# Kernel optimization log

Hardware: AMD Instinct MI355X
Metric: run time of the kernel (lower is better)

The kernel has to match this reference:

```python
import jax, jax.numpy as jnp
import numpy as np

NEG = -1e9  # matches torch masked_fill value (additive, not -inf)

def setup_inputs() -> dict:
    key = jax.random.key(0)
    k1, k2, k3, k4 = jax.random.split(key, 4)
    B, H, S, D = 8, 16, 1024, 64
    q = jax.random.normal(k1, (B, H, S, D), dtype=jnp.float32)
    k = jax.random.normal(k2, (B, H, S, D), dtype=jnp.float32)
    v = jax.random.normal(k3, (B, H, S, D), dtype=jnp.float32)
    event_length = jax.random.randint(k4, (B,), 0, S, dtype=jnp.int32)
    return {"q": q, "k": k, "v": v, "event_length": event_length}

def reference(q, k, v, event_length):
    B, H, S, D = q.shape
    scale = 1.0 / jnp.sqrt(jnp.asarray(D, dtype=q.dtype))
    idx = jnp.arange(S)
    # valid[b, i] = i < event_length[b]
    valid = idx[None, :] < event_length[:, None]            # [B, S]
    # additive mask: 0 where (row valid AND col valid), else -1e9
    pair = valid[:, :, None] & valid[:, None, :]            # [B, S, S]
    attn_mask = jnp.where(pair, 0.0, NEG).astype(q.dtype)[:, None, :, :]  # [B,1,S,S]
    scores = jnp.einsum('bhqd,bhkd->bhqk', q, k) * scale + attn_mask
    probs = jax.nn.softmax(scores, axis=-1)
    out = jnp.einsum('bhqk,bhkd->bhqd', probs, v)
    return out
```

## Files before the change

### kernel.cpp

```cpp
#include <hip/hip_runtime.h>


#define Sdim 1024
#define Ddim 64
#define PITCH 72

typedef float f32x4 __attribute__((ext_vector_type(4)));
typedef _Float16 f16x8 __attribute__((ext_vector_type(8)));
typedef unsigned short u16x8 __attribute__((ext_vector_type(8)));
typedef unsigned int u32x2 __attribute__((ext_vector_type(2)));

union FragU { u16x8 u; f16x8 h; };

__device__ __forceinline__ unsigned pk2(float a, float b) {
  auto h = __builtin_amdgcn_cvt_pkrtz(a, b);
  return __builtin_bit_cast(unsigned, h);
}

__device__ __forceinline__ float fexp2(float x) {
  float r;
  asm("v_exp_f32 %0, %1" : "=v"(r) : "v"(x));
  return r;
}

__global__ __launch_bounds__(256, 3)
void attn_fwd(const float* __restrict__ Q, const float* __restrict__ K,
              const float* __restrict__ V, const int* __restrict__ EL,
              float* __restrict__ Out) {
  __shared__ unsigned short k_lds[64 * PITCH];
  __shared__ unsigned short v_lds[64 * PITCH];
  __shared__ unsigned short p_lds[4][32 * PITCH];

  const int bid0 = blockIdx.x;
  const int x  = bid0 & 7;
  const int j  = bid0 >> 3;
  const int c  = j & 31;
  const int t  = j >> 5;
  const int p  = (c >> 2) + 8 * (t >> 1);
  const int i4 = c & 3;
  const int qt = (t & 1) ? (7 - i4) : i4;
  const int bh = p * 8 + x;
  const int L  = EL[bh >> 4];

  const int tid  = threadIdx.x;
  const size_t base = (size_t)bh * Sdim * Ddim;
  const float* Qb = Q + base;
  const float* Kb = K + base;
  const float* Vb = V + base;

  const int q0blk = qt * 128;

  if (q0blk >= L) {
    float* red = (float*)k_lds;
    const int sc4 = (tid & 15) * 4;
    const int rg0 = tid >> 4;
    const float* vp = Vb + (size_t)rg0 * Ddim + sc4;
    float4 acc = {0.f, 0.f, 0.f, 0.f};
#pragma unroll 8
    for (int i = 0; i < 64; ++i) {
      float4 a = *(const float4*)(vp + (size_t)i * 16 * Ddim);
      acc.x += a.x; acc.y += a.y; acc.z += a.z; acc.w += a.w;
    }
    *(float4*)&red[rg0 * 68 + sc4] = acc;
    __syncthreads();
    if (tid < 16) {
      float4 s = {0.f, 0.f, 0.f, 0.f};
#pragma unroll
      for (int i = 0; i < 16; ++i) {
        float4 a = *(const float4*)&red[i * 68 + tid * 4];
        s.x += a.x; s.y += a.y; s.z += a.z; s.w += a.w;
      }
      const float inv = 1.0f / 1024.0f;
      s.x *= inv; s.y *= inv; s.z *= inv; s.w *= inv;
      *(float4*)&red[16 * 68 + tid * 4] = s;
    }
    __syncthreads();
    const float4 cm = *(const float4*)&red[16 * 68 + sc4];
    float* ob = Out + base;
#pragma unroll
    for (int pp = 0; pp < 8; ++pp) {
      int row = q0blk + pp * 16 + rg0;
      *(float4*)&ob[(size_t)row * Ddim + sc4] = cm;
    }
    return;
  }

  const int w    = tid >> 6;
  const int lane = tid & 63;
  const int r    = lane & 15;
  const int hi   = lane >> 4;

  const int q0w      = q0blk + w * 32;
  const bool wValid  = q0w < L;
  const bool wAllVal = (q0w + 32) <= L;
  const int kFull    = (L + 63) >> 6;
  const int ktB      = L >> 6;

  const bool qv0 = (q0w + r) < L;
  const bool qv1 = (q0w + 16 + r) < L;
  const bool straddle = (q0blk + 128) > L;

  const float SCL = 0.125f * 1.44269504088896340736f;
  f16x8 qf[2][2];
  if (wValid) {
#pragma unroll
    for (int qc = 0; qc < 2; ++qc)
#pragma unroll
      for (int kk = 0; kk < 2; ++kk) {
        const float* pq = Qb + (size_t)(q0w + qc * 16 + r) * Ddim + kk * 32 + hi * 8;
        float4 a = *(const float4*)pq;
        float4 cc = *(const float4*)(pq + 4);
        union { unsigned u[4]; f16x8 h; } f;
        f.u[0] = pk2(a.x * SCL, a.y * SCL);  f.u[1] = pk2(a.z * SCL, a.w * SCL);
        f.u[2] = pk2(cc.x * SCL, cc.y * SCL); f.u[3] = pk2(cc.z * SCL, cc.w * SCL);
        qf[qc][kk] = f.h;
      }
  }

  const f32x4 zero4 = {0.f, 0.f, 0.f, 0.f};
  f32x4 oacc[2][4];
#pragma unroll
  for (int qc = 0; qc < 2; ++qc)
#pragma unroll
    for (int dc = 0; dc < 4; ++dc) oacc[qc][dc] = zero4;

  float lpart[2] = {0.f, 0.f};

  const int sr = tid >> 4, sc = tid & 15;
  const float* pK = Kb + (size_t)sr * Ddim + sc * 4;
  const float* pV = Vb + (size_t)(sr * 4) * Ddim + sc * 4;

  float4 kpre[4], vpre[4];
  auto LOADK = [&](int k0_) {
#pragma unroll
    for (int i = 0; i < 4; ++i)
      kpre[i] = *(const float4*)(pK + (size_t)(k0_ + 16 * i) * Ddim);
  };
  auto LOADV = [&](int k0_) {
#pragma unroll
    for (int jj = 0; jj < 4; ++jj)
      vpre[jj] = *(const float4*)(pV + (size_t)(k0_ + jj) * Ddim);
  };

  LOADK(0);
  LOADV(0);

  for (int kt = 0; kt < kFull; ++kt) {
    const int k0 = kt * 64;
    __syncthreads();

#pragma unroll
    for (int i = 0; i < 4; ++i) {
      u32x2 o;
      o[0] = pk2(kpre[i].x, kpre[i].y); o[1] = pk2(kpre[i].z, kpre[i].w);
      *(u32x2*)&k_lds[(16 * i + sr) * PITCH + sc * 4] = o;
    }
    {
      u32x2 o;
      o[0] = pk2(vpre[0].x, vpre[1].x); o[1] = pk2(vpre[2].x, vpre[3].x);
      *(u32x2*)&v_lds[(sc * 4 + 0) * PITCH + sr * 4] = o;
      o[0] = pk2(vpre[0].y, vpre[1].y); o[1] = pk2(vpre[2].y, vpre[3].y);
      *(u32x2*)&v_lds[(sc * 4 + 1) * PITCH + sr * 4] = o;
      o[0] = pk2(vpre[0].z, vpre[1].z); o[1] = pk2(vpre[2].z, vpre[3].z);
      *(u32x2*)&v_lds[(sc * 4 + 2) * PITCH + sr * 4] = o;
      o[0] = pk2(vpre[0].w, vpre[1].w); o[1] = pk2(vpre[2].w, vpre[3].w);
      *(u32x2*)&v_lds[(sc * 4 + 3) * PITCH + sr * 4] = o;
    }
    __syncthreads();

    if (kt + 1 < kFull) { LOADK(k0 + 64); LOADV(k0 + 64); }

    if (wValid) {
      f32x4 sacc[2][4];
#pragma unroll
      for (int qc = 0; qc < 2; ++qc)
#pragma unroll
        for (int kc = 0; kc < 4; ++kc) sacc[qc][kc] = zero4;

      __builtin_amdgcn_s_setprio(1);
#pragma unroll
      for (int kc = 0; kc < 4; ++kc)
#pragma unroll
        for (int kk = 0; kk < 2; ++kk) {
          FragU kf;
          kf.u = *(const u16x8*)&k_lds[(kc * 16 + r) * PITCH + kk * 32 + hi * 8];
          sacc[0][kc] = __builtin_amdgcn_mfma_f32_16x16x32_f16(kf.h, qf[0][kk], sacc[0][kc], 0, 0, 0);
          sacc[1][kc] = __builtin_amdgcn_mfma_f32_16x16x32_f16(kf.h, qf[1][kk], sacc[1][kc], 0, 0, 0);
        }
      __builtin_amdgcn_s_setprio(0);

      const bool noMask = wAllVal && (kt != ktB);
#pragma unroll
      for (int qc = 0; qc < 2; ++qc) {
        const bool qv = qc ? qv1 : qv0;
        float ls = 0.f;
#pragma unroll
        for (int kc = 0; kc < 4; ++kc) {
          float pr[4];
#pragma unroll
          for (int rg = 0; rg < 4; ++rg) {
            float s = sacc[qc][kc][rg];
            if (!noMask) {
              int kg = k0 + kc * 16 + 4 * hi + rg;
              s = (qv && kg < L) ? s : -__builtin_inff();
            }
            pr[rg] = fexp2(s);
            ls += pr[rg];
          }
          u32x2 o;
          o[0] = pk2(pr[0], pr[1]);
          o[1] = pk2(pr[2], pr[3]);
          *(u32x2*)&p_lds[w][(qc * 16 + r) * PITCH + kc * 16 + 4 * hi] = o;
        }
        lpart[qc] += ls;
      }

      asm volatile("s_waitcnt lgkmcnt(0)" ::: "memory");
      __builtin_amdgcn_sched_barrier(0);

      __builtin_amdgcn_s_setprio(1);
#pragma unroll
      for (int ks = 0; ks < 2; ++ks) {
        FragU pf0, pf1;
        pf0.u = *(const u16x8*)&p_lds[w][(0  + r) * PITCH + ks * 32 + hi * 8];
        pf1.u = *(const u16x8*)&p_lds[w][(16 + r) * PITCH + ks * 32 + hi * 8];
#pragma unroll
        for (int dc = 0; dc < 4; ++dc) {
          FragU vf;
          vf.u = *(const u16x8*)&v_lds[(dc * 16 + r) * PITCH + ks * 32 + hi * 8];
          oacc[0][dc] = __builtin_amdgcn_mfma_f32_16x16x32_f16(pf0.h, vf.h, oacc[0][dc], 0, 0, 0);
          oacc[1][dc] = __builtin_amdgcn_mfma_f32_16x16x32_f16(pf1.h, vf.h, oacc[1][dc], 0, 0, 0);
        }
      }
      __builtin_amdgcn_s_setprio(0);
    }
  }

  float* ob = Out + base;
#pragma unroll
  for (int qc = 0; qc < 2; ++qc) {
    float l = lpart[qc];
    l += __shfl_xor(l, 16, 64);
    l += __shfl_xor(l, 32, 64);
#pragma unroll
    for (int rg = 0; rg < 4; ++rg) {
      float lsq = __shfl(l, 4 * hi + rg, 64);
      float inv = 1.0f / lsq;
      int qrow = q0w + qc * 16 + 4 * hi + rg;
      if (qrow < L) {
#pragma unroll
        for (int dc = 0; dc < 4; ++dc)
          ob[(size_t)qrow * Ddim + dc * 16 + r] = oacc[qc][dc][rg] * inv;
      }
    }
  }

  if (straddle) {
    __syncthreads();
    float* red = (float*)k_lds;
    const int sc4 = (tid & 15) * 4;
    const int rg0 = tid >> 4;
    const float* vp = Vb + (size_t)rg0 * Ddim + sc4;
    float4 acc = {0.f, 0.f, 0.f, 0.f};
#pragma unroll 8
    for (int i = 0; i < 64; ++i) {
      float4 a = *(const float4*)(vp + (size_t)i * 16 * Ddim);
      acc.x += a.x; acc.y += a.y; acc.z += a.z; acc.w += a.w;
    }
    *(float4*)&red[rg0 * 68 + sc4] = acc;
    __syncthreads();
    if (tid < 16) {
      float4 s = {0.f, 0.f, 0.f, 0.f};
#pragma unroll
      for (int i = 0; i < 16; ++i) {
        float4 a = *(const float4*)&red[i * 68 + tid * 4];
        s.x += a.x; s.y += a.y; s.z += a.z; s.w += a.w;
      }
      const float inv = 1.0f / 1024.0f;
      s.x *= inv; s.y *= inv; s.z *= inv; s.w *= inv;
      *(float4*)&red[16 * 68 + tid * 4] = s;
    }
    __syncthreads();
    const float4 cm = *(const float4*)&red[16 * 68 + sc4];
#pragma unroll
    for (int pp = 0; pp < 8; ++pp) {
      int row = q0blk + pp * 16 + rg0;
      if (row >= L)
        *(float4*)&ob[(size_t)row * Ddim + sc4] = cm;
    }
  }
}

extern "C" void kernel_launch(void* const* d_in, const int* in_sizes, int n_in,
                              void* d_out, int out_size, void* d_ws, size_t ws_size,
                              hipStream_t stream) {
  const float* q  = (const float*)d_in[0];
  const float* k  = (const float*)d_in[1];
  const float* v  = (const float*)d_in[2];
  const int*   el = (const int*)d_in[3];
  float* out = (float*)d_out;
  dim3 grid(8 * 16 * (Sdim / 128));
  dim3 block(256);
  hipLaunchKernelGGL(attn_fwd, grid, block, 0, stream, q, k, v, el, out);
}
```

Measured before the change: 46.58 us.

## Halve query tile to 64 rows with 2-wave blocks and swizzle V LDS layout

Measured after the change: 51.29 us. 10.1% more time.

```diff
diff --git a/kernel.cpp b/kernel.cpp
--- a/kernel.cpp
+++ b/kernel.cpp
@@ -23,24 +23,21 @@
   return r;
 }
 
-__global__ __launch_bounds__(256, 3)
+__global__ __launch_bounds__(128, 2)
 void attn_fwd(const float* __restrict__ Q, const float* __restrict__ K,
               const float* __restrict__ V, const int* __restrict__ EL,
               float* __restrict__ Out) {
   __shared__ unsigned short k_lds[64 * PITCH];
   __shared__ unsigned short v_lds[64 * PITCH];
-  __shared__ unsigned short p_lds[4][32 * PITCH];
+  __shared__ unsigned short p_lds[2][32 * PITCH];
 
   const int bid0 = blockIdx.x;
-  const int x  = bid0 & 7;
-  const int j  = bid0 >> 3;
-  const int c  = j & 31;
-  const int t  = j >> 5;
-  const int p  = (c >> 2) + 8 * (t >> 1);
-  const int i4 = c & 3;
-  const int qt = (t & 1) ? (7 - i4) : i4;
-  const int bh = p * 8 + x;
-  const int L  = EL[bh >> 4];
+  const int x   = bid0 & 7;
+  const int j   = bid0 >> 3;
+  const int pan = j >> 4;
+  const int qt  = j & 15;
+  const int bh  = pan * 8 + x;
+  const int L   = EL[bh >> 4];
 
   const int tid  = threadIdx.x;
   const size_t base = (size_t)bh * Sdim * Ddim;
@@ -48,7 +45,7 @@
   const float* Kb = K + base;
   const float* Vb = V + base;
 
-  const int q0blk = qt * 128;
+  const int q0blk = qt * 64;
 
   if (q0blk >= L) {
     float* red = (float*)k_lds;
@@ -57,8 +54,8 @@
     const float* vp = Vb + (size_t)rg0 * Ddim + sc4;
     float4 acc = {0.f, 0.f, 0.f, 0.f};
 #pragma unroll 8
-    for (int i = 0; i < 64; ++i) {
-      float4 a = *(const float4*)(vp + (size_t)i * 16 * Ddim);
+    for (int i = 0; i < 128; ++i) {
+      float4 a = *(const float4*)(vp + (size_t)i * 8 * Ddim);
       acc.x += a.x; acc.y += a.y; acc.z += a.z; acc.w += a.w;
     }
     *(float4*)&red[rg0 * 68 + sc4] = acc;
@@ -66,20 +63,20 @@
     if (tid < 16) {
       float4 s = {0.f, 0.f, 0.f, 0.f};
 #pragma unroll
-      for (int i = 0; i < 16; ++i) {
+      for (int i = 0; i < 8; ++i) {
         float4 a = *(const float4*)&red[i * 68 + tid * 4];
         s.x += a.x; s.y += a.y; s.z += a.z; s.w += a.w;
       }
       const float inv = 1.0f / 1024.0f;
       s.x *= inv; s.y *= inv; s.z *= inv; s.w *= inv;
-      *(float4*)&red[16 * 68 + tid * 4] = s;
-    }
-    __syncthreads();
-    const float4 cm = *(const float4*)&red[16 * 68 + sc4];
+      *(float4*)&red[8 * 68 + tid * 4] = s;
+    }
+    __syncthreads();
+    const float4 cm = *(const float4*)&red[8 * 68 + sc4];
     float* ob = Out + base;
 #pragma unroll
     for (int pp = 0; pp < 8; ++pp) {
-      int row = q0blk + pp * 16 + rg0;
+      int row = q0blk + pp * 8 + rg0;
       *(float4*)&ob[(size_t)row * Ddim + sc4] = cm;
     }
     return;
@@ -89,16 +86,17 @@
   const int lane = tid & 63;
   const int r    = lane & 15;
   const int hi   = lane >> 4;
+  const int r3   = r >> 3;
 
   const int q0w      = q0blk + w * 32;
   const bool wValid  = q0w < L;
   const bool wAllVal = (q0w + 32) <= L;
   const int kFull    = (L + 63) >> 6;
   const int ktB      = L >> 6;
+  const bool straddle = (q0blk + 64) > L;
 
   const bool qv0 = (q0w + r) < L;
   const bool qv1 = (q0w + 16 + r) < L;
-  const bool straddle = (q0blk + 128) > L;
 
   const float SCL = 0.125f * 1.44269504088896340736f;
   f16x8 qf[2][2];
@@ -111,7 +109,7 @@
         float4 a = *(const float4*)pq;
         float4 cc = *(const float4*)(pq + 4);
         union { unsigned u[4]; f16x8 h; } f;
-        f.u[0] = pk2(a.x * SCL, a.y * SCL);  f.u[1] = pk2(a.z * SCL, a.w * SCL);
+        f.u[0] = pk2(a.x * SCL, a.y * SCL);   f.u[1] = pk2(a.z * SCL, a.w * SCL);
         f.u[2] = pk2(cc.x * SCL, cc.y * SCL); f.u[3] = pk2(cc.z * SCL, cc.w * SCL);
         qf[qc][kk] = f.h;
       }
@@ -126,20 +124,24 @@
 
   float lpart[2] = {0.f, 0.f};
 
-  const int sr = tid >> 4, sc = tid & 15;
+  const int sr = tid >> 4;
+  const int sc = tid & 15;
+  const int vskew = ((sc >> 1) & 7) * 8;
   const float* pK = Kb + (size_t)sr * Ddim + sc * 4;
   const float* pV = Vb + (size_t)(sr * 4) * Ddim + sc * 4;
 
-  float4 kpre[4], vpre[4];
+  float4 kpre[8], vpre[8];
   auto LOADK = [&](int k0_) {
 #pragma unroll
-    for (int i = 0; i < 4; ++i)
-      kpre[i] = *(const float4*)(pK + (size_t)(k0_ + 16 * i) * Ddim);
+    for (int i = 0; i < 8; ++i)
+      kpre[i] = *(const float4*)(pK + (size_t)(k0_ + 8 * i) * Ddim);
   };
   auto LOADV = [&](int k0_) {
 #pragma unroll
-    for (int jj = 0; jj < 4; ++jj)
-      vpre[jj] = *(const float4*)(pV + (size_t)(k0_ + jj) * Ddim);
+    for (int j2 = 0; j2 < 2; ++j2)
+#pragma unroll
+      for (int jj = 0; jj < 4; ++jj)
+        vpre[j2 * 4 + jj] = *(const float4*)(pV + (size_t)(k0_ + 32 * j2 + jj) * Ddim);
   };
 
   LOADK(0);
@@ -150,21 +152,23 @@
     __syncthreads();
 
 #pragma unroll
-    for (int i = 0; i < 4; ++i) {
+    for (int i = 0; i < 8; ++i) {
       u32x2 o;
       o[0] = pk2(kpre[i].x, kpre[i].y); o[1] = pk2(kpre[i].z, kpre[i].w);
-      *(u32x2*)&k_lds[(16 * i + sr) * PITCH + sc * 4] = o;
-    }
-    {
+      *(u32x2*)&k_lds[(8 * i + sr) * PITCH + sc * 4] = o;
+    }
+#pragma unroll
+    for (int j2 = 0; j2 < 2; ++j2) {
+      const int cp = (sr * 4 + 32 * j2 + vskew) & 63;
       u32x2 o;
-      o[0] = pk2(vpre[0].x, vpre[1].x); o[1] = pk2(vpre[2].x, vpre[3].x);
-      *(u32x2*)&v_lds[(sc * 4 + 0) * PITCH + sr * 4] = o;
-      o[0] = pk2(vpre[0].y, vpre[1].y); o[1] = pk2(vpre[2].y, vpre[3].y);
-      *(u32x2*)&v_lds[(sc * 4 + 1) * PITCH + sr * 4] = o;
-      o[0] = pk2(vpre[0].z, vpre[1].z); o[1] = pk2(vpre[2].z, vpre[3].z);
-      *(u32x2*)&v_lds[(sc * 4 + 2) * PITCH + sr * 4] = o;
-      o[0] = pk2(vpre[0].w, vpre[1].w); o[1] = pk2(vpre[2].w, vpre[3].w);
-      *(u32x2*)&v_lds[(sc * 4 + 3) * PITCH + sr * 4] = o;
+      o[0] = pk2(vpre[4*j2+0].x, vpre[4*j2+1].x); o[1] = pk2(vpre[4*j2+2].x, vpre[4*j2+3].x);
+      *(u32x2*)&v_lds[(sc * 4 + 0) * PITCH + cp] = o;
+      o[0] = pk2(vpre[4*j2+0].y, vpre[4*j2+1].y); o[1] = pk2(vpre[4*j2+2].y, vpre[4*j2+3].y);
+      *(u32x2*)&v_lds[(sc * 4 + 1) * PITCH + cp] = o;
+      o[0] = pk2(vpre[4*j2+0].z, vpre[4*j2+1].z); o[1] = pk2(vpre[4*j2+2].z, vpre[4*j2+3].z);
+      *(u32x2*)&v_lds[(sc * 4 + 2) * PITCH + cp] = o;
+      o[0] = pk2(vpre[4*j2+0].w, vpre[4*j2+1].w); o[1] = pk2(vpre[4*j2+2].w, vpre[4*j2+3].w);
+      *(u32x2*)&v_lds[(sc * 4 + 3) * PITCH + cp] = o;
     }
     __syncthreads();
 
@@ -226,8 +230,9 @@
         pf1.u = *(const u16x8*)&p_lds[w][(16 + r) * PITCH + ks * 32 + hi * 8];
 #pragma unroll
         for (int dc = 0; dc < 4; ++dc) {
+          const int vcp = (ks * 32 + hi * 8 + (((dc * 2 + r3) & 7) << 3)) & 63;
           FragU vf;
-          vf.u = *(const u16x8*)&v_lds[(dc * 16 + r) * PITCH + ks * 32 + hi * 8];
+          vf.u = *(const u16x8*)&v_lds[(dc * 16 + r) * PITCH + vcp];
           oacc[0][dc] = __builtin_amdgcn_mfma_f32_16x16x32_f16(pf0.h, vf.h, oacc[0][dc], 0, 0, 0);
           oacc[1][dc] = __builtin_amdgcn_mfma_f32_16x16x32_f16(pf1.h, vf.h, oacc[1][dc], 0, 0, 0);
         }
@@ -263,8 +268,8 @@
     const float* vp = Vb + (size_t)rg0 * Ddim + sc4;
     float4 acc = {0.f, 0.f, 0.f, 0.f};
 #pragma unroll 8
-    for (int i = 0; i < 64; ++i) {
-      float4 a = *(const float4*)(vp + (size_t)i * 16 * Ddim);
+    for (int i = 0; i < 128; ++i) {
+      float4 a = *(const float4*)(vp + (size_t)i * 8 * Ddim);
       acc.x += a.x; acc.y += a.y; acc.z += a.z; acc.w += a.w;
     }
     *(float4*)&red[rg0 * 68 + sc4] = acc;
@@ -272,19 +277,19 @@
     if (tid < 16) {
       float4 s = {0.f, 0.f, 0.f, 0.f};
 #pragma unroll
-      for (int i = 0; i < 16; ++i) {
+      for (int i = 0; i < 8; ++i) {
         float4 a = *(const float4*)&red[i * 68 + tid * 4];
         s.x += a.x; s.y += a.y; s.z += a.z; s.w += a.w;
       }
       const float inv = 1.0f / 1024.0f;
       s.x *= inv; s.y *= inv; s.z *= inv; s.w *= inv;
-      *(float4*)&red[16 * 68 + tid * 4] = s;
-    }
-    __syncthreads();
-    const float4 cm = *(const float4*)&red[16 * 68 + sc4];
+      *(float4*)&red[8 * 68 + tid * 4] = s;
+    }
+    __syncthreads();
+    const float4 cm = *(const float4*)&red[8 * 68 + sc4];
 #pragma unroll
     for (int pp = 0; pp < 8; ++pp) {
-      int row = q0blk + pp * 16 + rg0;
+      int row = q0blk + pp * 8 + rg0;
       if (row >= L)
         *(float4*)&ob[(size_t)row * Ddim + sc4] = cm;
     }
@@ -299,7 +304,7 @@
   const float* v  = (const float*)d_in[2];
   const int*   el = (const int*)d_in[3];
   float* out = (float*)d_out;
-  dim3 grid(8 * 16 * (Sdim / 128));
-  dim3 block(256);
+  dim3 grid(8 * 16 * (Sdim / 64));
+  dim3 block(128);
   hipLaunchKernelGGL(attn_fwd, grid, block, 0, stream, q, k, v, el, out);
 }
```

## Replace static tile grid with persistent blocks pulling work from atomic queues

Applied to the files above, without the earlier changes.

Result: slower. 101.9 us (+118.8%).

```diff
diff --git a/kernel.cpp b/kernel.cpp
--- a/kernel.cpp
+++ b/kernel.cpp
@@ -26,267 +26,277 @@
 __global__ __launch_bounds__(256, 3)
 void attn_fwd(const float* __restrict__ Q, const float* __restrict__ K,
               const float* __restrict__ V, const int* __restrict__ EL,
-              float* __restrict__ Out) {
+              float* __restrict__ Out, unsigned* __restrict__ queues) {
   __shared__ unsigned short k_lds[64 * PITCH];
   __shared__ unsigned short v_lds[64 * PITCH];
   __shared__ unsigned short p_lds[4][32 * PITCH];
-
-  const int bid0 = blockIdx.x;
-  const int x  = bid0 & 7;
-  const int j  = bid0 >> 3;
-  const int c  = j & 31;
-  const int t  = j >> 5;
-  const int p  = (c >> 2) + 8 * (t >> 1);
-  const int i4 = c & 3;
-  const int qt = (t & 1) ? (7 - i4) : i4;
-  const int bh = p * 8 + x;
-  const int L  = EL[bh >> 4];
-
-  const int tid  = threadIdx.x;
-  const size_t base = (size_t)bh * Sdim * Ddim;
-  const float* Qb = Q + base;
-  const float* Kb = K + base;
-  const float* Vb = V + base;
-
-  const int q0blk = qt * 128;
-
-  if (q0blk >= L) {
-    float* red = (float*)k_lds;
-    const int sc4 = (tid & 15) * 4;
-    const int rg0 = tid >> 4;
-    const float* vp = Vb + (size_t)rg0 * Ddim + sc4;
-    float4 acc = {0.f, 0.f, 0.f, 0.f};
-#pragma unroll 8
-    for (int i = 0; i < 64; ++i) {
-      float4 a = *(const float4*)(vp + (size_t)i * 16 * Ddim);
-      acc.x += a.x; acc.y += a.y; acc.z += a.z; acc.w += a.w;
-    }
-    *(float4*)&red[rg0 * 68 + sc4] = acc;
-    __syncthreads();
-    if (tid < 16) {
-      float4 s = {0.f, 0.f, 0.f, 0.f};
-#pragma unroll
-      for (int i = 0; i < 16; ++i) {
-        float4 a = *(const float4*)&red[i * 68 + tid * 4];
-        s.x += a.x; s.y += a.y; s.z += a.z; s.w += a.w;
-      }
-      const float inv = 1.0f / 1024.0f;
-      s.x *= inv; s.y *= inv; s.z *= inv; s.w *= inv;
-      *(float4*)&red[16 * 68 + tid * 4] = s;
-    }
-    __syncthreads();
-    const float4 cm = *(const float4*)&red[16 * 68 + sc4];
-    float* ob = Out + base;
-#pragma unroll
-    for (int pp = 0; pp < 8; ++pp) {
-      int row = q0blk + pp * 16 + rg0;
-      *(float4*)&ob[(size_t)row * Ddim + sc4] = cm;
-    }
-    return;
-  }
+  __shared__ int s_item;
+
+  const int tid   = threadIdx.x;
+  const int homeq = blockIdx.x & 7;
 
   const int w    = tid >> 6;
   const int lane = tid & 63;
   const int r    = lane & 15;
   const int hi   = lane >> 4;
-
-  const int q0w      = q0blk + w * 32;
-  const bool wValid  = q0w < L;
-  const bool wAllVal = (q0w + 32) <= L;
-  const int kFull    = (L + 63) >> 6;
-  const int ktB      = L >> 6;
-
-  const bool qv0 = (q0w + r) < L;
-  const bool qv1 = (q0w + 16 + r) < L;
-  const bool straddle = (q0blk + 128) > L;
-
-  const float SCL = 0.125f * 1.44269504088896340736f;
-  f16x8 qf[2][2];
-  if (wValid) {
-#pragma unroll
-    for (int qc = 0; qc < 2; ++qc)
-#pragma unroll
-      for (int kk = 0; kk < 2; ++kk) {
-        const float* pq = Qb + (size_t)(q0w + qc * 16 + r) * Ddim + kk * 32 + hi * 8;
-        float4 a = *(const float4*)pq;
-        float4 cc = *(const float4*)(pq + 4);
-        union { unsigned u[4]; f16x8 h; } f;
-        f.u[0] = pk2(a.x * SCL, a.y * SCL);  f.u[1] = pk2(a.z * SCL, a.w * SCL);
-        f.u[2] = pk2(cc.x * SCL, cc.y * SCL); f.u[3] = pk2(cc.z * SCL, cc.w * SCL);
-        qf[qc][kk] = f.h;
-      }
-  }
-
-  const f32x4 zero4 = {0.f, 0.f, 0.f, 0.f};
-  f32x4 oacc[2][4];
-#pragma unroll
-  for (int qc = 0; qc < 2; ++qc)
-#pragma unroll
-    for (int dc = 0; dc < 4; ++dc) oacc[qc][dc] = zero4;
-
-  float lpart[2] = {0.f, 0.f};
-
-  const int sr = tid >> 4, sc = tid & 15;
-  const float* pK = Kb + (size_t)sr * Ddim + sc * 4;
-  const float* pV = Vb + (size_t)(sr * 4) * Ddim + sc * 4;
-
-  float4 kpre[4], vpre[4];
-  auto LOADK = [&](int k0_) {
-#pragma unroll
-    for (int i = 0; i < 4; ++i)
-      kpre[i] = *(const float4*)(pK + (size_t)(k0_ + 16 * i) * Ddim);
-  };
-  auto LOADV = [&](int k0_) {
-#pragma unroll
-    for (int jj = 0; jj < 4; ++jj)
-      vpre[jj] = *(const float4*)(pV + (size_t)(k0_ + jj) * Ddim);
-  };
-
-  LOADK(0);
-  LOADV(0);
-
-  for (int kt = 0; kt < kFull; ++kt) {
-    const int k0 = kt * 64;
-    __syncthreads();
-
-#pragma unroll
-    for (int i = 0; i < 4; ++i) {
-      u32x2 o;
-      o[0] = pk2(kpre[i].x, kpre[i].y); o[1] = pk2(kpre[i].z, kpre[i].w);
-      *(u32x2*)&k_lds[(16 * i + sr) * PITCH + sc * 4] = o;
-    }
-    {
-      u32x2 o;
-      o[0] = pk2(vpre[0].x, vpre[1].x); o[1] = pk2(vpre[2].x, vpre[3].x);
-      *(u32x2*)&v_lds[(sc * 4 + 0) * PITCH + sr * 4] = o;
-      o[0] = pk2(vpre[0].y, vpre[1].y); o[1] = pk2(vpre[2].y, vpre[3].y);
-      *(u32x2*)&v_lds[(sc * 4 + 1) * PITCH + sr * 4] = o;
-      o[0] = pk2(vpre[0].z, vpre[1].z); o[1] = pk2(vpre[2].z, vpre[3].z);
-      *(u32x2*)&v_lds[(sc * 4 + 2) * PITCH + sr * 4] = o;
-      o[0] = pk2(vpre[0].w, vpre[1].w); o[1] = pk2(vpre[2].w, vpre[3].w);
-      *(u32x2*)&v_lds[(sc * 4 + 3) * PITCH + sr * 4] = o;
-    }
-    __syncthreads();
-
-    if (kt + 1 < kFull) { LOADK(k0 + 64); LOADV(k0 + 64); }
-
-    if (wValid) {
-      f32x4 sacc[2][4];
+  const int r3   = r >> 3;
+  const int sr   = tid >> 4;
+  const int sc   = tid & 15;
+  const int vskew = ((sc >> 1) & 7) * 8;
+
+  for (int qsel = 0; qsel < 8; ++qsel) {
+    const int h = (homeq + qsel) & 7;
+    for (;;) {
+      __syncthreads();
+      if (tid == 0) s_item = (int)atomicAdd(&queues[h], 1u);
+      __syncthreads();
+      const int g = s_item;
+      if (g >= 128) break;
+
+      const int pan = g >> 3;
+      const int qt  = g & 7;
+      const int bh  = pan * 8 + h;
+      const int L   = EL[bh >> 4];
+
+      const size_t base = (size_t)bh * Sdim * Ddim;
+      const float* Qb = Q + base;
+      const float* Kb = K + base;
+      const float* Vb = V + base;
+      float* ob = Out + base;
+
+      const int q0blk = qt * 128;
+
+      if (q0blk >= L) {
+        float* red = (float*)k_lds;
+        const int sc4 = sc * 4;
+        const float* vp = Vb + (size_t)sr * Ddim + sc4;
+        float4 acc = {0.f, 0.f, 0.f, 0.f};
+#pragma unroll 8
+        for (int i = 0; i < 64; ++i) {
+          float4 a = *(const float4*)(vp + (size_t)i * 16 * Ddim);
+          acc.x += a.x; acc.y += a.y; acc.z += a.z; acc.w += a.w;
+        }
+        *(float4*)&red[sr * 68 + sc4] = acc;
+        __syncthreads();
+        if (tid < 16) {
+          float4 s = {0.f, 0.f, 0.f, 0.f};
+#pragma unroll
+          for (int i = 0; i < 16; ++i) {
+            float4 a = *(const float4*)&red[i * 68 + tid * 4];
+            s.x += a.x; s.y += a.y; s.z += a.z; s.w += a.w;
+          }
+          const float inv = 1.0f / 1024.0f;
+          s.x *= inv; s.y *= inv; s.z *= inv; s.w *= inv;
+          *(float4*)&red[16 * 68 + tid * 4] = s;
+        }
+        __syncthreads();
+        const float4 cm = *(const float4*)&red[16 * 68 + sc4];
+#pragma unroll
+        for (int pp = 0; pp < 8; ++pp) {
+          int row = q0blk + pp * 16 + sr;
+          *(float4*)&ob[(size_t)row * Ddim + sc4] = cm;
+        }
+        continue;
+      }
+
+      const int q0w      = q0blk + w * 32;
+      const bool wValid  = q0w < L;
+      const bool wAllVal = (q0w + 32) <= L;
+      const int kFull    = (L + 63) >> 6;
+      const int ktB      = L >> 6;
+      const bool straddle = (q0blk + 128) > L;
+
+      const bool qv0 = (q0w + r) < L;
+      const bool qv1 = (q0w + 16 + r) < L;
+
+      const float SCL = 0.125f * 1.44269504088896340736f;
+      f16x8 qf[2][2];
+      if (wValid) {
+#pragma unroll
+        for (int qc = 0; qc < 2; ++qc)
+#pragma unroll
+          for (int kk = 0; kk < 2; ++kk) {
+            const float* pq = Qb + (size_t)(q0w + qc * 16 + r) * Ddim + kk * 32 + hi * 8;
+            float4 a = *(const float4*)pq;
+            float4 cc = *(const float4*)(pq + 4);
+            union { unsigned u[4]; f16x8 hh; } f;
+            f.u[0] = pk2(a.x * SCL, a.y * SCL);   f.u[1] = pk2(a.z * SCL, a.w * SCL);
+            f.u[2] = pk2(cc.x * SCL, cc.y * SCL); f.u[3] = pk2(cc.z * SCL, cc.w * SCL);
+            qf[qc][kk] = f.hh;
+          }
+      }
+
+      const f32x4 zero4 = {0.f, 0.f, 0.f, 0.f};
+      f32x4 oacc[2][4];
 #pragma unroll
       for (int qc = 0; qc < 2; ++qc)
 #pragma unroll
-        for (int kc = 0; kc < 4; ++kc) sacc[qc][kc] = zero4;
-
-      __builtin_amdgcn_s_setprio(1);
-#pragma unroll
-      for (int kc = 0; kc < 4; ++kc)
-#pragma unroll
-        for (int kk = 0; kk < 2; ++kk) {
-          FragU kf;
-          kf.u = *(const u16x8*)&k_lds[(kc * 16 + r) * PITCH + kk * 32 + hi * 8];
-          sacc[0][kc] = __builtin_amdgcn_mfma_f32_16x16x32_f16(kf.h, qf[0][kk], sacc[0][kc], 0, 0, 0);
-          sacc[1][kc] = __builtin_amdgcn_mfma_f32_16x16x32_f16(kf.h, qf[1][kk], sacc[1][kc], 0, 0, 0);
-        }
-      __builtin_amdgcn_s_setprio(0);
-
-      const bool noMask = wAllVal && (kt != ktB);
+        for (int dc = 0; dc < 4; ++dc) oacc[qc][dc] = zero4;
+
+      float lpart[2] = {0.f, 0.f};
+
+      const float* pK = Kb + (size_t)sr * Ddim + sc * 4;
+      const float* pV = Vb + (size_t)(sr * 4) * Ddim + sc * 4;
+
+      float4 kpre[4], vpre[4];
+      auto LOADK = [&](int k0_) {
+#pragma unroll
+        for (int i = 0; i < 4; ++i)
+          kpre[i] = *(const float4*)(pK + (size_t)(k0_ + 16 * i) * Ddim);
+      };
+      auto LOADV = [&](int k0_) {
+#pragma unroll
+        for (int jj = 0; jj < 4; ++jj)
+          vpre[jj] = *(const float4*)(pV + (size_t)(k0_ + jj) * Ddim);
+      };
+
+      LOADK(0);
+      LOADV(0);
+
+      for (int kt = 0; kt < kFull; ++kt) {
+        const int k0 = kt * 64;
+        __syncthreads();
+
+#pragma unroll
+        for (int i = 0; i < 4; ++i) {
+          u32x2 o;
+          o[0] = pk2(kpre[i].x, kpre[i].y); o[1] = pk2(kpre[i].z, kpre[i].w);
+          *(u32x2*)&k_lds[(16 * i + sr) * PITCH + sc * 4] = o;
+        }
+        {
+          const int cp = (sr * 4 + vskew) & 63;
+          u32x2 o;
+          o[0] = pk2(vpre[0].x, vpre[1].x); o[1] = pk2(vpre[2].x, vpre[3].x);
+          *(u32x2*)&v_lds[(sc * 4 + 0) * PITCH + cp] = o;
+          o[0] = pk2(vpre[0].y, vpre[1].y); o[1] = pk2(vpre[2].y, vpre[3].y);
+          *(u32x2*)&v_lds[(sc * 4 + 1) * PITCH + cp] = o;
+          o[0] = pk2(vpre[0].z, vpre[1].z); o[1] = pk2(vpre[2].z, vpre[3].z);
+          *(u32x2*)&v_lds[(sc * 4 + 2) * PITCH + cp] = o;
+          o[0] = pk2(vpre[0].w, vpre[1].w); o[1] = pk2(vpre[2].w, vpre[3].w);
+          *(u32x2*)&v_lds[(sc * 4 + 3) * PITCH + cp] = o;
+        }
+        __syncthreads();
+
+        if (kt + 1 < kFull) { LOADK(k0 + 64); LOADV(k0 + 64); }
+
+        if (wValid) {
+          f32x4 sacc[2][4];
+#pragma unroll
+          for (int qc = 0; qc < 2; ++qc)
+#pragma unroll
+            for (int kc = 0; kc < 4; ++kc) sacc[qc][kc] = zero4;
+
+          __builtin_amdgcn_s_setprio(1);
+#pragma unroll
+          for (int kc = 0; kc < 4; ++kc)
+#pragma unroll
+            for (int kk = 0; kk < 2; ++kk) {
+              FragU kf;
+              kf.u = *(const u16x8*)&k_lds[(kc * 16 + r) * PITCH + kk * 32 + hi * 8];
+              sacc[0][kc] = __builtin_amdgcn_mfma_f32_16x16x32_f16(kf.h, qf[0][kk], sacc[0][kc], 0, 0, 0);
+              sacc[1][kc] = __builtin_amdgcn_mfma_f32_16x16x32_f16(kf.h, qf[1][kk], sacc[1][kc], 0, 0, 0);
+            }
+          __builtin_amdgcn_s_setprio(0);
+
+          const bool noMask = wAllVal && (kt != ktB);
+#pragma unroll
+          for (int qc = 0; qc < 2; ++qc) {
+            const bool qv = qc ? qv1 : qv0;
+            float ls = 0.f;
+#pragma unroll
+            for (int kc = 0; kc < 4; ++kc) {
+              float pr[4];
+#pragma unroll
+              for (int rg = 0; rg < 4; ++rg) {
+                float s = sacc[qc][kc][rg];
+                if (!noMask) {
+                  int kg = k0 + kc * 16 + 4 * hi + rg;
+                  s = (qv && kg < L) ? s : -__builtin_inff();
+                }
+                pr[rg] = fexp2(s);
+                ls += pr[rg];
+              }
+              u32x2 o;
+              o[0] = pk2(pr[0], pr[1]);
+              o[1] = pk2(pr[2], pr[3]);
+              *(u32x2*)&p_lds[w][(qc * 16 + r) * PITCH + kc * 16 + 4 * hi] = o;
+            }
+            lpart[qc] += ls;
+          }
+
+          asm volatile("s_waitcnt lgkmcnt(0)" ::: "memory");
+          __builtin_amdgcn_sched_barrier(0);
+
+          __builtin_amdgcn_s_setprio(1);
+#pragma unroll
+          for (int ks = 0; ks < 2; ++ks) {
+            FragU pf0, pf1;
+            pf0.u = *(const u16x8*)&p_lds[w][(0  + r) * PITCH + ks * 32 + hi * 8];
+            pf1.u = *(const u16x8*)&p_lds[w][(16 + r) * PITCH + ks * 32 + hi * 8];
+#pragma unroll
+            for (int dc = 0; dc < 4; ++dc) {
+              const int vcp = (ks * 32 + hi * 8 + (((dc * 2 + r3) & 7) << 3)) & 63;
+              FragU vf;
+              vf.u = *(const u16x8*)&v_lds[(dc * 16 + r) * PITCH + vcp];
+              oacc[0][dc] = __builtin_amdgcn_mfma_f32_16x16x32_f16(pf0.h, vf.h, oacc[0][dc], 0, 0, 0);
+              oacc[1][dc] = __builtin_amdgcn_mfma_f32_16x16x32_f16(pf1.h, vf.h, oacc[1][dc], 0, 0, 0);
+            }
+          }
+          __builtin_amdgcn_s_setprio(0);
+        }
+      }
+
 #pragma unroll
       for (int qc = 0; qc < 2; ++qc) {
-        const bool qv = qc ? qv1 : qv0;
-        float ls = 0.f;
-#pragma unroll
-        for (int kc = 0; kc < 4; ++kc) {
-          float pr[4];
-#pragma unroll
-          for (int rg = 0; rg < 4; ++rg) {
-            float s = sacc[qc][kc][rg];
-            if (!noMask) {
-              int kg = k0 + kc * 16 + 4 * hi + rg;
-              s = (qv && kg < L) ? s : -__builtin_inff();
-            }
-            pr[rg] = fexp2(s);
-            ls += pr[rg];
-          }
-          u32x2 o;
-          o[0] = pk2(pr[0], pr[1]);
-          o[1] = pk2(pr[2], pr[3]);
-          *(u32x2*)&p_lds[w][(qc * 16 + r) * PITCH + kc * 16 + 4 * hi] = o;
-        }
-        lpart[qc] += ls;
-      }
-
-      asm volatile("s_waitcnt lgkmcnt(0)" ::: "memory");
-      __builtin_amdgcn_sched_barrier(0);
-
-      __builtin_amdgcn_s_setprio(1);
-#pragma unroll
-      for (int ks = 0; ks < 2; ++ks) {
-        FragU pf0, pf1;
-        pf0.u = *(const u16x8*)&p_lds[w][(0  + r) * PITCH + ks * 32 + hi * 8];
-        pf1.u = *(const u16x8*)&p_lds[w][(16 + r) * PITCH + ks * 32 + hi * 8];
-#pragma unroll
-        for (int dc = 0; dc < 4; ++dc) {
-          FragU vf;
-          vf.u = *(const u16x8*)&v_lds[(dc * 16 + r) * PITCH + ks * 32 + hi * 8];
-          oacc[0][dc] = __builtin_amdgcn_mfma_f32_16x16x32_f16(pf0.h, vf.h, oacc[0][dc], 0, 0, 0);
-          oacc[1][dc] = __builtin_amdgcn_mfma_f32_16x16x32_f16(pf1.h, vf.h, oacc[1][dc], 0, 0, 0);
-        }
-      }
-      __builtin_amdgcn_s_setprio(0);
-    }
-  }
-
-  float* ob = Out + base;
-#pragma unroll
-  for (int qc = 0; qc < 2; ++qc) {
-    float l = lpart[qc];
-    l += __shfl_xor(l, 16, 64);
-    l += __shfl_xor(l, 32, 64);
-#pragma unroll
-    for (int rg = 0; rg < 4; ++rg) {
-      float lsq = __shfl(l, 4 * hi + rg, 64);
-      float inv = 1.0f / lsq;
-      int qrow = q0w + qc * 16 + 4 * hi + rg;
-      if (qrow < L) {
-#pragma unroll
-        for (int dc = 0; dc < 4; ++dc)
-          ob[(size_t)qrow * Ddim + dc * 16 + r] = oacc[qc][dc][rg] * inv;
-      }
-    }
-  }
-
-  if (straddle) {
-    __syncthreads();
-    float* red = (float*)k_lds;
-    const int sc4 = (tid & 15) * 4;
-    const int rg0 = tid >> 4;
-    const float* vp = Vb + (size_t)rg0 * Ddim + sc4;
-    float4 acc = {0.f, 0.f, 0.f, 0.f};
+        float l = lpart[qc];
+        l += __shfl_xor(l, 16, 64);
+        l += __shfl_xor(l, 32, 64);
+#pragma unroll
+        for (int rg = 0; rg < 4; ++rg) {
+          float lsq = __shfl(l, 4 * hi + rg, 64);
+          float inv = 1.0f / lsq;
+          int qrow = q0w + qc * 16 + 4 * hi + rg;
+          if (qrow < L) {
+#pragma unroll
+            for (int dc = 0; dc < 4; ++dc)
+              ob[(size_t)qrow * Ddim + dc * 16 + r] = oacc[qc][dc][rg] * inv;
+          }
+        }
+      }
+
+      if (straddle) {
+        __syncthreads();
+        float* red = (float*)k_lds;
+        const int sc4 = sc * 4;
+        const float* vp = Vb + (size_t)sr * Ddim + sc4;
+        float4 acc = {0.f, 0.f, 0.f, 0.f};
 #pragma unroll 8
-    for (int i = 0; i < 64; ++i) {
-      float4 a = *(const float4*)(vp + (size_t)i * 16 * Ddim);
-      acc.x += a.x; acc.y += a.y; acc.z += a.z; acc.w += a.w;
-    }
-    *(float4*)&red[rg0 * 68 + sc4] = acc;
-    __syncthreads();
-    if (tid < 16) {
-      float4 s = {0.f, 0.f, 0.f, 0.f};
-#pragma unroll
-      for (int i = 0; i < 16; ++i) {
-        float4 a = *(const float4*)&red[i * 68 + tid * 4];
-        s.x += a.x; s.y += a.y; s.z += a.z; s.w += a.w;
-      }
-      const float inv = 1.0f / 1024.0f;
-      s.x *= inv; s.y *= inv; s.z *= inv; s.w *= inv;
-      *(float4*)&red[16 * 68 + tid * 4] = s;
-    }
-    __syncthreads();
-    const float4 cm = *(const float4*)&red[16 * 68 + sc4];
-#pragma unroll
-    for (int pp = 0; pp < 8; ++pp) {
-      int row = q0blk + pp * 16 + rg0;
-      if (row >= L)
-        *(float4*)&ob[(size_t)row * Ddim + sc4] = cm;
+        for (int i = 0; i < 64; ++i) {
+          float4 a = *(const float4*)(vp + (size_t)i * 16 * Ddim);
+          acc.x += a.x; acc.y += a.y; acc.z += a.z; acc.w += a.w;
+        }
+        *(float4*)&red[sr * 68 + sc4] = acc;
+        __syncthreads();
+        if (tid < 16) {
+          float4 s = {0.f, 0.f, 0.f, 0.f};
+#pragma unroll
+          for (int i = 0; i < 16; ++i) {
+            float4 a = *(const float4*)&red[i * 68 + tid * 4];
+            s.x += a.x; s.y += a.y; s.z += a.z; s.w += a.w;
+          }
+          const float inv = 1.0f / 1024.0f;
+          s.x *= inv; s.y *= inv; s.z *= inv; s.w *= inv;
+          *(float4*)&red[16 * 68 + tid * 4] = s;
+        }
+        __syncthreads();
+        const float4 cm = *(const float4*)&red[16 * 68 + sc4];
+#pragma unroll
+        for (int pp = 0; pp < 8; ++pp) {
+          int row = q0blk + pp * 16 + sr;
+          if (row >= L)
+            *(float4*)&ob[(size_t)row * Ddim + sc4] = cm;
+        }
+      }
     }
   }
 }
@@ -299,7 +309,9 @@
   const float* v  = (const float*)d_in[2];
   const int*   el = (const int*)d_in[3];
   float* out = (float*)d_out;
-  dim3 grid(8 * 16 * (Sdim / 128));
+  hipMemsetAsync(d_ws, 0, 64, stream);
+  dim3 grid(768);
   dim3 block(256);
-  hipLaunchKernelGGL(attn_fwd, grid, block, 0, stream, q, k, v, el, out);
+  hipLaunchKernelGGL(attn_fwd, grid, block, 0, stream, q, k, v, el, out,
+                     (unsigned*)d_ws);
 }
```
